# Optimization experiments

Hardware: AMD Instinct MI355X
Metric: run time of the kernel (lower is better)

Reference implementation:

```python
import jax, jax.numpy as jnp
import numpy as np

TOPOLOGY = [-1, 0, 0, 0, 1, 2, 3, 4, 5, 6, 7, 8, 9, 9, 9, 12, 13, 14, 16, 17, 18, 19, 20, 21]
JOINT_WEIGHTS = np.ones(24, dtype=np.float32)
B1 = 1.0
B2 = 1.0


def quaternion_to_matrix(q):
    # pytorch3d convention: real part first (w, x, y, z)
    w, x, y, z = q[..., 0], q[..., 1], q[..., 2], q[..., 3]
    two_s = 2.0 / jnp.sum(q * q, axis=-1)
    o = jnp.stack([
        1 - two_s * (y * y + z * z), two_s * (x * y - z * w), two_s * (x * z + y * w),
        two_s * (x * y + z * w), 1 - two_s * (x * x + z * z), two_s * (y * z - x * w),
        two_s * (x * z - y * w), two_s * (y * z + x * w), 1 - two_s * (x * x + y * y),
    ], axis=-1)
    return o.reshape(q.shape[:-1] + (3, 3))


def fk(topology, X_m, X_t):
    # X_m: (bs, T, J*4+3), X_t: (bs, J, 3)
    J = len(topology)
    quat = X_m[..., :-3].reshape(X_m.shape[:-1] + (J, 4))
    local_rot = quaternion_to_matrix(quat)          # (bs, T, J, 3, 3)
    grots = [None] * J
    gtrs = [None] * J
    grots[0] = local_rot[..., 0, :, :]
    gtrs[0] = X_m[..., -3:]                          # root translation
    for i in range(1, J):
        pi = topology[i]
        grots[i] = jnp.matmul(grots[pi], local_rot[..., i, :, :])
        gtrs[i] = jnp.einsum('btij,bj->bti', grots[pi], X_t[:, i]) + gtrs[pi]
    return jnp.stack(grots, axis=-3), jnp.stack(gtrs, axis=-2)


def split_raw_motion(raw_motion):
    position = raw_motion[..., -3:]
    rotation = raw_motion[..., :-3]
    rotation = rotation.reshape(rotation.shape[:-1] + (-1, 4))
    norm = jnp.linalg.norm(rotation, axis=-1, keepdims=True)
    rotation = rotation / jnp.maximum(norm, 1e-12)
    return rotation, position


def weighted_mse(w, a, b):
    # w: (J,), a/b: (bs, T, J, C) -> per-joint weighted mean squared error
    return jnp.mean(w[None, None, :, None] * (a - b) ** 2)


def setup_inputs() -> dict:
    key = jax.random.key(0)
    k1, k2, k3, k4 = jax.random.split(key, 4)
    bs, T, J = 64, 2048, 24
    return {
        'Y_m': jax.random.normal(k1, (bs, T, J * 4 + 3), dtype=jnp.float32),
        'X_m': jax.random.normal(k2, (bs, T, J * 4 + 3), dtype=jnp.float32),
        'Y_t': jax.random.normal(k3, (bs, J, 3), dtype=jnp.float32),
        'X_t': jax.random.normal(k4, (bs, J, 3), dtype=jnp.float32),
    }


def reference(Y_m, X_m, Y_t, X_t):
    w = jnp.asarray(JOINT_WEIGHTS)
    rot_x, pos_x = split_raw_motion(X_m)
    rot_y, pos_y = split_raw_motion(Y_m)
    grot_y, gtr_y = fk(TOPOLOGY, Y_m, Y_t)
    grot_x, gtr_x = fk(TOPOLOGY, X_m, X_t)
    loss_rot = B1 * weighted_mse(w, rot_y, rot_x)
    loss_fk = B2 * (2.5 * weighted_mse(w, gtr_y, gtr_x)
                    + jnp.mean((pos_y - pos_x) ** 2))
    return loss_rot + loss_fk
```

## Files before the change

kernel.cpp:

```cpp
#include <hip/hip_runtime.h>

#define NJ 24
#define ROWF 99
#define BS 64
#define TT 2048
#define NROWS (BS * TT)
#define TROWS 32
#define BLOCK 64
#define NBLOCKS (NROWS / TROWS)
#define TILE4 (TROWS * ROWF / 4)

__device__ __forceinline__ void quat2mat(float w, float x, float y, float z, float* R) {
  float s = 2.0f / (w*w + x*x + y*y + z*z);
  float xx = s*x*x, yy = s*y*y, zz = s*z*z;
  float xy = s*x*y, xz = s*x*z, yz = s*y*z;
  float xw = s*x*w, yw = s*y*w, zw = s*z*w;
  R[0] = 1.0f - (yy+zz); R[1] = xy - zw;        R[2] = xz + yw;
  R[3] = xy + zw;        R[4] = 1.0f - (xx+zz); R[5] = yz - xw;
  R[6] = xz - yw;        R[7] = yz + xw;        R[8] = 1.0f - (xx+yy);
}

__device__ __forceinline__ void mm3(const float* A, const float* B, float* C) {
#pragma unroll
  for (int r = 0; r < 3; ++r)
#pragma unroll
    for (int c = 0; c < 3; ++c)
      C[3*r+c] = fmaf(A[3*r], B[c], fmaf(A[3*r+1], B[3+c], A[3*r+2]*B[6+c]));
}

#define QMSE(q0, q1, q2, q3) ({ \
  float _n  = sqrtf((q0)*(q0) + (q1)*(q1) + (q2)*(q2) + (q3)*(q3)); \
  float _iv = 1.0f / fmaxf(_n, 1e-12f); \
  float _a0 = (q0)*_iv, _a1 = (q1)*_iv, _a2 = (q2)*_iv, _a3 = (q3)*_iv; \
  float _d0 = _a0 - __shfl_xor(_a0, 1, 64); \
  float _d1 = _a1 - __shfl_xor(_a1, 1, 64); \
  float _d2 = _a2 - __shfl_xor(_a2, 1, 64); \
  float _d3 = _a3 - __shfl_xor(_a3, 1, 64); \
  _d0*_d0 + _d1*_d1 + _d2*_d2 + _d3*_d3; })

#define TDIFF(t0, t1, t2) ({ \
  float _e0 = (t0) - __shfl_xor((t0), 1, 64); \
  float _e1 = (t1) - __shfl_xor((t1), 1, 64); \
  float _e2 = (t2) - __shfl_xor((t2), 1, 64); \
  _e0*_e0 + _e1*_e1 + _e2*_e2; })

#define STEP(c, GP, TP, GO, TO) do { \
  float q0 = rowp[4*(c)], q1 = rowp[4*(c)+1], q2 = rowp[4*(c)+2], q3 = rowp[4*(c)+3]; \
  rot_acc += QMSE(q0, q1, q2, q3); \
  float R[9]; quat2mat(q0, q1, q2, q3, R); \
  mm3(GP, R, GO); \
  float v0 = tv[3*(c)], v1 = tv[3*(c)+1], v2 = tv[3*(c)+2]; \
  TO[0] = fmaf(GP[0], v0, fmaf(GP[1], v1, fmaf(GP[2], v2, TP[0]))); \
  TO[1] = fmaf(GP[3], v0, fmaf(GP[4], v1, fmaf(GP[5], v2, TP[1]))); \
  TO[2] = fmaf(GP[6], v0, fmaf(GP[7], v1, fmaf(GP[8], v2, TP[2]))); \
  gacc += TDIFF(TO[0], TO[1], TO[2]); \
} while (0)

#define LEAF(c, GP, TP) do { \
  float q0 = rowp[4*(c)], q1 = rowp[4*(c)+1], q2 = rowp[4*(c)+2], q3 = rowp[4*(c)+3]; \
  rot_acc += QMSE(q0, q1, q2, q3); \
  float v0 = tv[3*(c)], v1 = tv[3*(c)+1], v2 = tv[3*(c)+2]; \
  float t0 = fmaf(GP[0], v0, fmaf(GP[1], v1, fmaf(GP[2], v2, TP[0]))); \
  float t1 = fmaf(GP[3], v0, fmaf(GP[4], v1, fmaf(GP[5], v2, TP[1]))); \
  float t2 = fmaf(GP[6], v0, fmaf(GP[7], v1, fmaf(GP[8], v2, TP[2]))); \
  gacc += TDIFF(t0, t1, t2); \
} while (0)

__global__ __launch_bounds__(BLOCK, 2) void motion_loss_kernel(
    const float* __restrict__ Ym, const float* __restrict__ Xm,
    const float* __restrict__ Yt, const float* __restrict__ Xt,
    float* __restrict__ out) {
  __shared__ __align__(16) float tX[TROWS * ROWF];
  __shared__ __align__(16) float tY[TROWS * ROWF];
  __shared__ float tvX[NJ * 3], tvY[NJ * 3];

  const int lane = threadIdx.x;
  const int blk = blockIdx.x;
  const size_t row0 = (size_t)blk * TROWS;
  const int b = (int)(row0 >> 11);

  const float4* gx = (const float4*)(Xm + row0 * ROWF);
  const float4* gy = (const float4*)(Ym + row0 * ROWF);
  float4* lx4 = (float4*)tX;
  float4* ly4 = (float4*)tY;
  {
    float4 r0[6], r1[6];
#pragma unroll
    for (int k = 0; k < 6; ++k) r0[k] = gx[k * BLOCK + lane];
#pragma unroll
    for (int k = 0; k < 6; ++k) r1[k] = gy[k * BLOCK + lane];
#pragma unroll
    for (int k = 0; k < 6; ++k) lx4[k * BLOCK + lane] = r0[k];
#pragma unroll
    for (int k = 0; k < 6; ++k) ly4[k * BLOCK + lane] = r1[k];
#pragma unroll
    for (int k = 0; k < 6; ++k) r0[k] = gx[(6 + k) * BLOCK + lane];
#pragma unroll
    for (int k = 0; k < 6; ++k) r1[k] = gy[(6 + k) * BLOCK + lane];
#pragma unroll
    for (int k = 0; k < 6; ++k) lx4[(6 + k) * BLOCK + lane] = r0[k];
#pragma unroll
    for (int k = 0; k < 6; ++k) ly4[(6 + k) * BLOCK + lane] = r1[k];
    if (lane < TILE4 - 12 * BLOCK) {
      lx4[12 * BLOCK + lane] = gx[12 * BLOCK + lane];
      ly4[12 * BLOCK + lane] = gy[12 * BLOCK + lane];
    }
  }
#pragma unroll
  for (int k = 0; k < 3; ++k) {
    int id = k * BLOCK + lane;
    if (id < 72) tvX[id] = Xt[(size_t)b * 72 + id];
    else if (id < 144) tvY[id - 72] = Yt[(size_t)b * 72 + (id - 72)];
  }
  __syncthreads();

  const int par = lane & 1;
  const int rl  = lane >> 1;
  const float* __restrict__ rowp = (par ? tY : tX) + rl * ROWF;
  const float* __restrict__ tv   = par ? tvY : tvX;

  float rot_acc = 0.0f, gacc = 0.0f;
  float GA[9], GB[9], GC[9], GD[9];
  float TA[3], TB[3], TC[3], TD[3];

  {
    float q0 = rowp[0], q1 = rowp[1], q2 = rowp[2], q3 = rowp[3];
    rot_acc += QMSE(q0, q1, q2, q3);
    quat2mat(q0, q1, q2, q3, GA);
  }
  TA[0] = rowp[96]; TA[1] = rowp[97]; TA[2] = rowp[98];
  float rootd2 = TDIFF(TA[0], TA[1], TA[2]);
  gacc += rootd2;

  STEP(1,  GA, TA, GB, TB);
  STEP(2,  GA, TA, GC, TC);
  STEP(3,  GA, TA, GD, TD);
  STEP(4,  GB, TB, GA, TA);
  STEP(5,  GC, TC, GB, TB);
  STEP(6,  GD, TD, GC, TC);
  STEP(7,  GA, TA, GD, TD);
  STEP(8,  GB, TB, GA, TA);
  STEP(9,  GC, TC, GB, TB);
  LEAF(10, GD, TD);
  LEAF(11, GA, TA);
  STEP(12, GB, TB, GC, TC);
  STEP(13, GB, TB, GD, TD);
  STEP(14, GB, TB, GA, TA);
  LEAF(15, GC, TC);
  STEP(16, GD, TD, GB, TB);
  STEP(17, GA, TA, GC, TC);
  STEP(18, GB, TB, GD, TD);
  STEP(19, GC, TC, GA, TA);
  STEP(20, GD, TD, GB, TB);
  STEP(21, GA, TA, GC, TC);
  LEAF(22, GB, TB);
  LEAF(23, GC, TC);

  const float c_rot = 1.0f / ((float)NROWS * NJ * 4);
  const float c_gtr = 2.5f / ((float)NROWS * NJ * 3);
  const float c_pos = 1.0f / ((float)NROWS * 3);
  float contrib = 0.5f * (c_rot * rot_acc + c_gtr * gacc + c_pos * rootd2);
#pragma unroll
  for (int o = 32; o > 0; o >>= 1) contrib += __shfl_down(contrib, o, 64);
  if (lane == 0) atomicAdd(out, contrib);
}

extern "C" void kernel_launch(void* const* d_in, const int* in_sizes, int n_in,
                              void* d_out, int out_size, void* d_ws, size_t ws_size,
                              hipStream_t stream) {
  const float* Ym = (const float*)d_in[0];
  const float* Xm = (const float*)d_in[1];
  const float* Yt = (const float*)d_in[2];
  const float* Xt = (const float*)d_in[3];
  float* out = (float*)d_out;
  hipMemsetAsync(out, 0, sizeof(float), stream);
  motion_loss_kernel<<<NBLOCKS, BLOCK, 0, stream>>>(Ym, Xm, Yt, Xt, out);
}
```

Before: 175.9 us.

## Stream quaternion tiles via global_load_lds double buffering with transposed LDS layout

Loads each block's quaternion data in three 32-float chunks straight into LDS with global_load_lds, double-buffered so later chunks arrive while earlier joints are processed. The tile is stored column-major (component-major per row), which avoids bank conflicts from the 99-float row stride. Root positions are read directly from global memory, and LDS per block shrinks enough to raise launch bounds to 4 blocks. The cost is extra barriers and scalar 4-byte loads with a strided global pattern in place of coalesced float4 loads.

```diff
diff --git a/kernel.cpp b/kernel.cpp
--- a/kernel.cpp
+++ b/kernel.cpp
@@ -2,13 +2,29 @@
 
 #define NJ 24
 #define ROWF 99
-#define BS 64
 #define TT 2048
-#define NROWS (BS * TT)
+#define NROWS (64 * 2048)
 #define TROWS 32
 #define BLOCK 64
 #define NBLOCKS (NROWS / TROWS)
-#define TILE4 (TROWS * ROWF / 4)
+
+template<int OFF>
+__device__ __forceinline__ void glds4(const float* gp, float* lp) {
+  __builtin_amdgcn_global_load_lds(
+      (const __attribute__((address_space(1))) void*)gp,
+      (__attribute__((address_space(3))) void*)lp, 4, OFF, 0);
+}
+
+#define GI(C, S, I)                                                  \
+  glds4<(C)*128 + (I)*8>(axg, &buf[S][0][(I)*64]);                   \
+  glds4<(C)*128 + (I)*8>(ayg, &buf[S][1][(I)*64]);
+
+#define ISSUE_CHUNK(C, S) do {                                       \
+  GI(C, S, 0)  GI(C, S, 1)  GI(C, S, 2)  GI(C, S, 3)                 \
+  GI(C, S, 4)  GI(C, S, 5)  GI(C, S, 6)  GI(C, S, 7)                 \
+  GI(C, S, 8)  GI(C, S, 9)  GI(C, S, 10) GI(C, S, 11)                \
+  GI(C, S, 12) GI(C, S, 13) GI(C, S, 14) GI(C, S, 15)                \
+} while (0)
 
 __device__ __forceinline__ void quat2mat(float w, float x, float y, float z, float* R) {
   float s = 2.0f / (w*w + x*x + y*y + z*z);
@@ -44,8 +60,9 @@
   float _e2 = (t2) - __shfl_xor((t2), 1, 64); \
   _e0*_e0 + _e1*_e1 + _e2*_e2; })
 
-#define STEP(c, GP, TP, GO, TO) do { \
-  float q0 = rowp[4*(c)], q1 = rowp[4*(c)+1], q2 = rowp[4*(c)+2], q3 = rowp[4*(c)+3]; \
+#define STEP(qb, c, cc, GP, TP, GO, TO) do { \
+  float q0 = (qb)[(((cc)*4+0)<<5) + rr], q1 = (qb)[(((cc)*4+1)<<5) + rr]; \
+  float q2 = (qb)[(((cc)*4+2)<<5) + rr], q3 = (qb)[(((cc)*4+3)<<5) + rr]; \
   rot_acc += QMSE(q0, q1, q2, q3); \
   float R[9]; quat2mat(q0, q1, q2, q3, R); \
   mm3(GP, R, GO); \
@@ -56,8 +73,9 @@
   gacc += TDIFF(TO[0], TO[1], TO[2]); \
 } while (0)
 
-#define LEAF(c, GP, TP) do { \
-  float q0 = rowp[4*(c)], q1 = rowp[4*(c)+1], q2 = rowp[4*(c)+2], q3 = rowp[4*(c)+3]; \
+#define LEAF(qb, c, cc, GP, TP) do { \
+  float q0 = (qb)[(((cc)*4+0)<<5) + rr], q1 = (qb)[(((cc)*4+1)<<5) + rr]; \
+  float q2 = (qb)[(((cc)*4+2)<<5) + rr], q3 = (qb)[(((cc)*4+3)<<5) + rr]; \
   rot_acc += QMSE(q0, q1, q2, q3); \
   float v0 = tv[3*(c)], v1 = tv[3*(c)+1], v2 = tv[3*(c)+2]; \
   float t0 = fmaf(GP[0], v0, fmaf(GP[1], v1, fmaf(GP[2], v2, TP[0]))); \
@@ -66,46 +84,28 @@
   gacc += TDIFF(t0, t1, t2); \
 } while (0)
 
-__global__ __launch_bounds__(BLOCK, 2) void motion_loss_kernel(
+__global__ __launch_bounds__(BLOCK, 4) void motion_loss_kernel(
     const float* __restrict__ Ym, const float* __restrict__ Xm,
     const float* __restrict__ Yt, const float* __restrict__ Xt,
     float* __restrict__ out) {
-  __shared__ __align__(16) float tX[TROWS * ROWF];
-  __shared__ __align__(16) float tY[TROWS * ROWF];
-  __shared__ float tvX[NJ * 3], tvY[NJ * 3];
+  __shared__ float buf[2][2][1024];
+  __shared__ float tvX[72], tvY[72];
 
   const int lane = threadIdx.x;
-  const int blk = blockIdx.x;
-  const size_t row0 = (size_t)blk * TROWS;
+  const size_t row0 = (size_t)blockIdx.x * TROWS;
   const int b = (int)(row0 >> 11);
 
-  const float4* gx = (const float4*)(Xm + row0 * ROWF);
-  const float4* gy = (const float4*)(Ym + row0 * ROWF);
-  float4* lx4 = (float4*)tX;
-  float4* ly4 = (float4*)tY;
-  {
-    float4 r0[6], r1[6];
-#pragma unroll
-    for (int k = 0; k < 6; ++k) r0[k] = gx[k * BLOCK + lane];
-#pragma unroll
-    for (int k = 0; k < 6; ++k) r1[k] = gy[k * BLOCK + lane];
-#pragma unroll
-    for (int k = 0; k < 6; ++k) lx4[k * BLOCK + lane] = r0[k];
-#pragma unroll
-    for (int k = 0; k < 6; ++k) ly4[k * BLOCK + lane] = r1[k];
-#pragma unroll
-    for (int k = 0; k < 6; ++k) r0[k] = gx[(6 + k) * BLOCK + lane];
-#pragma unroll
-    for (int k = 0; k < 6; ++k) r1[k] = gy[(6 + k) * BLOCK + lane];
-#pragma unroll
-    for (int k = 0; k < 6; ++k) lx4[(6 + k) * BLOCK + lane] = r0[k];
-#pragma unroll
-    for (int k = 0; k < 6; ++k) ly4[(6 + k) * BLOCK + lane] = r1[k];
-    if (lane < TILE4 - 12 * BLOCK) {
-      lx4[12 * BLOCK + lane] = gx[12 * BLOCK + lane];
-      ly4[12 * BLOCK + lane] = gy[12 * BLOCK + lane];
-    }
-  }
+  const int Pf = (lane & 31) * ROWF + (lane >> 5);
+  const float* axg = Xm + row0 * ROWF + Pf;
+  const float* ayg = Ym + row0 * ROWF + Pf;
+
+  const int par = lane & 1;
+  const int rr  = lane >> 1;
+
+  const float* posp = (par ? Ym : Xm) + (row0 + rr) * ROWF + 96;
+  float p0 = posp[0], p1 = posp[1], p2 = posp[2];
+
+  ISSUE_CHUNK(0, 0);
 #pragma unroll
   for (int k = 0; k < 3; ++k) {
     int id = k * BLOCK + lane;
@@ -113,48 +113,54 @@
     else if (id < 144) tvY[id - 72] = Yt[(size_t)b * 72 + (id - 72)];
   }
   __syncthreads();
+  ISSUE_CHUNK(1, 1);
 
-  const int par = lane & 1;
-  const int rl  = lane >> 1;
-  const float* __restrict__ rowp = (par ? tY : tX) + rl * ROWF;
-  const float* __restrict__ tv   = par ? tvY : tvX;
+  const float* tv  = par ? tvY : tvX;
+  const float* qb0 = &buf[0][0][0] + par * 1024;
+  const float* qb1 = &buf[1][0][0] + par * 1024;
 
   float rot_acc = 0.0f, gacc = 0.0f;
   float GA[9], GB[9], GC[9], GD[9];
   float TA[3], TB[3], TC[3], TD[3];
 
   {
-    float q0 = rowp[0], q1 = rowp[1], q2 = rowp[2], q3 = rowp[3];
+    float q0 = qb0[(0<<5)+rr], q1 = qb0[(1<<5)+rr];
+    float q2 = qb0[(2<<5)+rr], q3 = qb0[(3<<5)+rr];
     rot_acc += QMSE(q0, q1, q2, q3);
     quat2mat(q0, q1, q2, q3, GA);
   }
-  TA[0] = rowp[96]; TA[1] = rowp[97]; TA[2] = rowp[98];
+  TA[0] = p0; TA[1] = p1; TA[2] = p2;
   float rootd2 = TDIFF(TA[0], TA[1], TA[2]);
   gacc += rootd2;
 
-  STEP(1,  GA, TA, GB, TB);
-  STEP(2,  GA, TA, GC, TC);
-  STEP(3,  GA, TA, GD, TD);
-  STEP(4,  GB, TB, GA, TA);
-  STEP(5,  GC, TC, GB, TB);
-  STEP(6,  GD, TD, GC, TC);
-  STEP(7,  GA, TA, GD, TD);
-  STEP(8,  GB, TB, GA, TA);
-  STEP(9,  GC, TC, GB, TB);
-  LEAF(10, GD, TD);
-  LEAF(11, GA, TA);
-  STEP(12, GB, TB, GC, TC);
-  STEP(13, GB, TB, GD, TD);
-  STEP(14, GB, TB, GA, TA);
-  LEAF(15, GC, TC);
-  STEP(16, GD, TD, GB, TB);
-  STEP(17, GA, TA, GC, TC);
-  STEP(18, GB, TB, GD, TD);
-  STEP(19, GC, TC, GA, TA);
-  STEP(20, GD, TD, GB, TB);
-  STEP(21, GA, TA, GC, TC);
-  LEAF(22, GB, TB);
-  LEAF(23, GC, TC);
+  STEP(qb0, 1, 1, GA, TA, GB, TB);
+  STEP(qb0, 2, 2, GA, TA, GC, TC);
+  STEP(qb0, 3, 3, GA, TA, GD, TD);
+  STEP(qb0, 4, 4, GB, TB, GA, TA);
+  STEP(qb0, 5, 5, GC, TC, GB, TB);
+  STEP(qb0, 6, 6, GD, TD, GC, TC);
+  STEP(qb0, 7, 7, GA, TA, GD, TD);
+  __syncthreads();
+  ISSUE_CHUNK(2, 0);
+
+  STEP(qb1,  8, 0, GB, TB, GA, TA);
+  STEP(qb1,  9, 1, GC, TC, GB, TB);
+  LEAF(qb1, 10, 2, GD, TD);
+  LEAF(qb1, 11, 3, GA, TA);
+  STEP(qb1, 12, 4, GB, TB, GC, TC);
+  STEP(qb1, 13, 5, GB, TB, GD, TD);
+  STEP(qb1, 14, 6, GB, TB, GA, TA);
+  LEAF(qb1, 15, 7, GC, TC);
+  __syncthreads();
+
+  STEP(qb0, 16, 0, GD, TD, GB, TB);
+  STEP(qb0, 17, 1, GA, TA, GC, TC);
+  STEP(qb0, 18, 2, GB, TB, GD, TD);
+  STEP(qb0, 19, 3, GC, TC, GA, TA);
+  STEP(qb0, 20, 4, GD, TD, GB, TB);
+  STEP(qb0, 21, 5, GA, TA, GC, TC);
+  LEAF(qb0, 22, 6, GB, TB);
+  LEAF(qb0, 23, 7, GC, TC);
 
   const float c_rot = 1.0f / ((float)NROWS * NJ * 4);
   const float c_gtr = 2.5f / ((float)NROWS * NJ * 3);
@@ -173,6 +179,6 @@
   const float* Yt = (const float*)d_in[2];
   const float* Xt = (const float*)d_in[3];
   float* out = (float*)d_out;
-  hipMemsetAsync(out, 0, sizeof(float), stream);
+  (void)hipMemsetAsync(out, 0, sizeof(float), stream);
   motion_loss_kernel<<<NBLOCKS, BLOCK, 0, stream>>>(Ym, Xm, Yt, Xt, out);
 }
```

Result: slower. 207.2 us (+17.8%).
